# Optimization experiments

Hardware: AMD Instinct MI355X
Metric: run time of the kernel (lower is better)

The kernel has to match this reference:

```python
import jax, jax.numpy as jnp
import numpy as np

K = 64      # neighbor_num (subgraph size)
TOPK = 10   # topk for sparse adjacency scatter
DN = 10     # density_neighbor


def _build_graphs(indexes, features):
    # compute_knn: inner-product top-K neighbor table over all N samples
    N, D = features.shape
    sim = features @ features.T                      # [N, N]
    _, ori0 = jax.lax.top_k(sim, K)                  # [N, K] neighbor indices
    # density: all_sim[n] = sum_{i<DN} <f_n, f_{ori0[n,i]}> / (4*DN)
    g = features[ori0[:, :DN]]                       # [N, DN, D]
    all_sim = jnp.einsum('nd,nkd->n', features, g) / (4.0 * DN)
    exp_sim = jnp.exp(all_sim)                       # [N]

    rows = jnp.arange(K)[:, None]                    # [K,1]

    def build_one(idx):
        nbr = ori0[idx]                              # [K] neighbors of query idx
        feat = features[nbr]                         # [K, D]
        neigh = ori0[nbr][:, :TOPK]                  # [K, TOPK]
        A = (feat @ features.T) * exp_sim[None, :]   # [K, N] density-reweighted sims
        # scatter only the topk entries of each row into sparse tmp
        tmp = jnp.zeros((K, N), features.dtype).at[rows, neigh].set(A[rows, neigh])
        adj = tmp @ (tmp.T > 0).astype(features.dtype)   # [K, K]
        adj = jax.nn.softmax(adj, axis=1)
        x = feat - feat[0]                           # center on query node
        return x, adj

    return jax.vmap(build_one)(indexes)              # [B,K,D], [B,K,K]


def _gconv(x, adj, W, b):
    # GraphConv with MeanAggregator: out = relu(concat([x, adj@x]) @ W + b)
    agg = jnp.einsum('bij,bjd->bid', adj, x)
    cat = jnp.concatenate([x, agg], axis=-1)
    return jax.nn.relu(jnp.einsum('bkd,df->bkf', cat, W) + b)


def setup_inputs() -> dict:
    key = jax.random.key(0)
    ks = jax.random.split(key, 16)
    N, D, NHID = 8192, 2048, 1024
    feats = jax.random.normal(ks[0], (N, D), dtype=jnp.float32)
    feats = feats / jnp.linalg.norm(feats, axis=1, keepdims=True)  # L2-normalized embeddings
    p = lambda k, shape: jax.random.normal(k, shape, dtype=jnp.float32) * 0.02
    return {
        'indexes': jax.random.randint(ks[1], (64,), 0, N, dtype=jnp.int64) if jax.config.jax_enable_x64 else jax.random.randint(ks[1], (64,), 0, N, dtype=jnp.int32),
        'features': feats,
        'labels': jax.random.randint(ks[2], (N,), 0, 1000, dtype=jnp.int32),
        'domain': 1,
        'W1': p(ks[3], (2 * D, NHID)), 'b1': jnp.zeros((NHID,), jnp.float32),
        'W2': p(ks[4], (2 * NHID, 512)), 'b2': jnp.zeros((512,), jnp.float32),
        'W3': p(ks[5], (2 * 512, 256)), 'b3': jnp.zeros((256,), jnp.float32),
        'W4': p(ks[6], (2 * 256, 256)), 'b4': jnp.zeros((256,), jnp.float32),
        'Wc1': p(ks[7], (256, 256)), 'bc1': jnp.zeros((256,), jnp.float32),
        'prelu_a': jnp.full((256,), 0.25, jnp.float32),
        'Wc2': p(ks[8], (256, 2)), 'bc2': jnp.zeros((2,), jnp.float32),
    }


def reference(indexes, features, labels, domain, W1, b1, W2, b2, W3, b3, W4, b4,
              Wc1, bc1, prelu_a, Wc2, bc2):
    # labels only used for the (optional) loss branch; domain=1 path implemented.
    xs, adjs = _build_graphs(indexes, features)      # built under no_grad in torch
    h = _gconv(xs, adjs, W1, b1)
    h = _gconv(h, adjs, W2, b2)
    h = _gconv(h, adjs, W3, b3)
    h = _gconv(h, adjs, W4, b4)
    h = h @ Wc1 + bc1
    h = jnp.where(h > 0, h, prelu_a * h)             # PReLU(256)
    pred = h @ Wc2 + bc2                             # [B, K, 2]
    return pred
```

## Files before the change

kernel.cpp:

```cpp
#include <hip/hip_runtime.h>
#include <hip/hip_bf16.h>
#include <math.h>

#define NROWS 8192
#define DFEAT 2048
#define KSEL  64
#define CHK   2048

typedef unsigned long long u64;
typedef __attribute__((ext_vector_type(8))) short bf16x8;
typedef __attribute__((ext_vector_type(4))) float f32x4;

__device__ __forceinline__ u64 umax64(u64 a, u64 b) { return a > b ? a : b; }

__device__ __forceinline__ void split2(float v, ushort& h, ushort& l) {
  __hip_bfloat16 bh = __float2bfloat16(v);
  float r = v - __bfloat162float(bh);
  __hip_bfloat16 bl = __float2bfloat16(r);
  h = *(ushort*)&bh; l = *(ushort*)&bl;
}

__device__ __forceinline__ u64 mkkey_vi(float v, int i) {
  unsigned u = __float_as_uint(v);
  u = ((int)u < 0) ? ~u : (u | 0x80000000u);
  return ((u64)u << 32) | (u64)(0xFFFFFFFFu - (unsigned)i);
}

__global__ __launch_bounds__(256) void k_split(const float* __restrict__ F, ushort* __restrict__ H,
                                               ushort* __restrict__ M, ushort* __restrict__ L) {
  const size_t i0 = ((size_t)blockIdx.x * 256 + threadIdx.x) * 4;
  float4 x = *(const float4*)(F + i0);
  float xs[4] = {x.x, x.y, x.z, x.w};
  ushort h[4], m[4], l[4];
#pragma unroll
  for (int c = 0; c < 4; ++c) {
    float v = xs[c];
    __hip_bfloat16 bh = __float2bfloat16(v);
    float r1 = v - __bfloat162float(bh);
    __hip_bfloat16 bm = __float2bfloat16(r1);
    float r2 = r1 - __bfloat162float(bm);
    __hip_bfloat16 bl = __float2bfloat16(r2);
    h[c] = *(ushort*)&bh; m[c] = *(ushort*)&bm; l[c] = *(ushort*)&bl;
  }
  ushort4 vh = {h[0], h[1], h[2], h[3]};
  ushort4 vm = {m[0], m[1], m[2], m[3]};
  ushort4 vl = {l[0], l[1], l[2], l[3]};
  *(ushort4*)(H + i0) = vh;
  *(ushort4*)(M + i0) = vm;
  *(ushort4*)(L + i0) = vl;
}

__global__ __launch_bounds__(256) void k_simgemm_diag(
    const ushort* __restrict__ FH, const ushort* __restrict__ FM, const ushort* __restrict__ FL,
    float* __restrict__ bufbase) {
  __shared__ ushort lds[6 * 4096];
  const int cc = blockIdx.z;
  const int bj = blockIdx.x;
  const int bm = blockIdx.y;
  if (bm > bj) return;
  float* TILE = bufbase + (size_t)cc * CHK * CHK;
  const int t = threadIdx.x;
  const int w = t >> 6, l = t & 63;
  const int arow0 = cc * CHK + bm * 128;
  const int brow0 = cc * CHK + bj * 128;
  const int segr = l >> 2;
  const int segq_s = (l & 3) ^ ((l >> 3) & 3);
  const int fl15 = l & 15, fq = l >> 4;
  const int kswz = (fq ^ ((fl15 >> 1) & 3)) * 8;
  const int wr = w >> 1, wc = w & 1;
  const int mb = wr * 64, nb = wc * 64;

  f32x4 acc[4][4];
#pragma unroll
  for (int i = 0; i < 4; ++i)
#pragma unroll
    for (int j = 0; j < 4; ++j) acc[i][j] = (f32x4){0.f, 0.f, 0.f, 0.f};

  for (int k0 = 0; k0 < DFEAT; k0 += 32) {
    __syncthreads();
#pragma unroll
    for (int c = 0; c < 12; ++c) {
      const int cidx = w * 12 + c;
      const int tt = cidx >> 3;
      const int p = cidx & 7;
      const int rowbase = (tt < 3) ? arow0 : brow0;
      const int sp = (tt < 3) ? tt : (tt - 3);
      const ushort* sel = (sp == 0) ? FH : ((sp == 1) ? FM : FL);
      const ushort* g = sel + (size_t)(rowbase + p * 16 + segr) * DFEAT + (k0 + segq_s * 8);
      __builtin_amdgcn_global_load_lds((const __attribute__((address_space(1))) unsigned int*)g,
                                       (__attribute__((address_space(3))) unsigned int*)&lds[tt * 4096 + p * 512],
                                       16, 0, 0);
    }
    __syncthreads();

    bf16x8 af[3][4];
    bf16x8 bg[3][4];
#pragma unroll
    for (int i = 0; i < 3; ++i)
#pragma unroll
      for (int fm = 0; fm < 4; ++fm)
        af[i][fm] = *(const bf16x8*)&lds[i * 4096 + (mb + fm * 16 + fl15) * 32 + kswz];
#pragma unroll
    for (int j = 0; j < 3; ++j)
#pragma unroll
      for (int fn = 0; fn < 4; ++fn)
        bg[j][fn] = *(const bf16x8*)&lds[(3 + j) * 4096 + (nb + fn * 16 + fl15) * 32 + kswz];

#pragma unroll
    for (int fm = 0; fm < 4; ++fm)
#pragma unroll
      for (int fn = 0; fn < 4; ++fn) {
        f32x4 a = acc[fm][fn];
        a = __builtin_amdgcn_mfma_f32_16x16x32_bf16(af[0][fm], bg[0][fn], a, 0, 0, 0);
        a = __builtin_amdgcn_mfma_f32_16x16x32_bf16(af[1][fm], bg[0][fn], a, 0, 0, 0);
        a = __builtin_amdgcn_mfma_f32_16x16x32_bf16(af[0][fm], bg[1][fn], a, 0, 0, 0);
        a = __builtin_amdgcn_mfma_f32_16x16x32_bf16(af[2][fm], bg[0][fn], a, 0, 0, 0);
        a = __builtin_amdgcn_mfma_f32_16x16x32_bf16(af[0][fm], bg[2][fn], a, 0, 0, 0);
        a = __builtin_amdgcn_mfma_f32_16x16x32_bf16(af[1][fm], bg[1][fn], a, 0, 0, 0);
        acc[fm][fn] = a;
      }
  }

  const bool doT = (bm != bj);
#pragma unroll
  for (int fm = 0; fm < 4; ++fm) {
    const int lm = bm * 128 + mb + fm * 16 + fq * 4;
#pragma unroll
    for (int fn = 0; fn < 4; ++fn) {
      const int col = bj * 128 + nb + fn * 16 + fl15;
#pragma unroll
      for (int r = 0; r < 4; ++r)
        TILE[(size_t)(lm + r) * CHK + col] = acc[fm][fn][r];
      if (doT) {
        float4 v = make_float4(acc[fm][fn][0], acc[fm][fn][1], acc[fm][fn][2], acc[fm][fn][3]);
        *(float4*)(TILE + (size_t)col * CHK + lm) = v;
      }
    }
  }
}

__global__ __launch_bounds__(256) void k_simgemm_pair(
    const ushort* __restrict__ FH, const ushort* __restrict__ FM, const ushort* __restrict__ FL,
    float* __restrict__ T0, float* __restrict__ T0T, int i0, int j0,
    float* __restrict__ T1, float* __restrict__ T1T, int i1, int j1) {
  __shared__ ushort lds[6 * 4096];
  const int z = blockIdx.z;
  float* TILE = z ? T1 : T0;
  float* TILT = z ? T1T : T0T;
  const int ci = z ? i1 : i0;
  const int cj = z ? j1 : j0;
  const int bj = blockIdx.x;
  const int bm = blockIdx.y;
  const int t = threadIdx.x;
  const int w = t >> 6, l = t & 63;
  const int arow0 = ci * CHK + bm * 128;
  const int brow0 = cj * CHK + bj * 128;
  const int segr = l >> 2;
  const int segq_s = (l & 3) ^ ((l >> 3) & 3);
  const int fl15 = l & 15, fq = l >> 4;
  const int kswz = (fq ^ ((fl15 >> 1) & 3)) * 8;
  const int wr = w >> 1, wc = w & 1;
  const int mb = wr * 64, nb = wc * 64;

  f32x4 acc[4][4];
#pragma unroll
  for (int i = 0; i < 4; ++i)
#pragma unroll
    for (int j = 0; j < 4; ++j) acc[i][j] = (f32x4){0.f, 0.f, 0.f, 0.f};

  for (int k0 = 0; k0 < DFEAT; k0 += 32) {
    __syncthreads();
#pragma unroll
    for (int c = 0; c < 12; ++c) {
      const int cc = w * 12 + c;
      const int tt = cc >> 3;
      const int p = cc & 7;
      const int rowbase = (tt < 3) ? arow0 : brow0;
      const int sp = (tt < 3) ? tt : (tt - 3);
      const ushort* sel = (sp == 0) ? FH : ((sp == 1) ? FM : FL);
      const ushort* g = sel + (size_t)(rowbase + p * 16 + segr) * DFEAT + (k0 + segq_s * 8);
      __builtin_amdgcn_global_load_lds((const __attribute__((address_space(1))) unsigned int*)g,
                                       (__attribute__((address_space(3))) unsigned int*)&lds[tt * 4096 + p * 512],
                                       16, 0, 0);
    }
    __syncthreads();

    bf16x8 af[3][4];
    bf16x8 bg[3][4];
#pragma unroll
    for (int i = 0; i < 3; ++i)
#pragma unroll
      for (int fm = 0; fm < 4; ++fm)
        af[i][fm] = *(const bf16x8*)&lds[i * 4096 + (mb + fm * 16 + fl15) * 32 + kswz];
#pragma unroll
    for (int j = 0; j < 3; ++j)
#pragma unroll
      for (int fn = 0; fn < 4; ++fn)
        bg[j][fn] = *(const bf16x8*)&lds[(3 + j) * 4096 + (nb + fn * 16 + fl15) * 32 + kswz];

#pragma unroll
    for (int fm = 0; fm < 4; ++fm)
#pragma unroll
      for (int fn = 0; fn < 4; ++fn) {
        f32x4 a = acc[fm][fn];
        a = __builtin_amdgcn_mfma_f32_16x16x32_bf16(af[0][fm], bg[0][fn], a, 0, 0, 0);
        a = __builtin_amdgcn_mfma_f32_16x16x32_bf16(af[1][fm], bg[0][fn], a, 0, 0, 0);
        a = __builtin_amdgcn_mfma_f32_16x16x32_bf16(af[0][fm], bg[1][fn], a, 0, 0, 0);
        a = __builtin_amdgcn_mfma_f32_16x16x32_bf16(af[2][fm], bg[0][fn], a, 0, 0, 0);
        a = __builtin_amdgcn_mfma_f32_16x16x32_bf16(af[0][fm], bg[2][fn], a, 0, 0, 0);
        a = __builtin_amdgcn_mfma_f32_16x16x32_bf16(af[1][fm], bg[1][fn], a, 0, 0, 0);
        acc[fm][fn] = a;
      }
  }

#pragma unroll
  for (int fm = 0; fm < 4; ++fm) {
    const int lm = bm * 128 + mb + fm * 16 + fq * 4;
#pragma unroll
    for (int fn = 0; fn < 4; ++fn) {
      const int col = bj * 128 + nb + fn * 16 + fl15;
#pragma unroll
      for (int r = 0; r < 4; ++r)
        TILE[(size_t)(lm + r) * CHK + col] = acc[fm][fn][r];
      float4 v = make_float4(acc[fm][fn][0], acc[fm][fn][1], acc[fm][fn][2], acc[fm][fn][3]);
      *(float4*)(TILT + (size_t)col * CHK + lm) = v;
    }
  }
}

__global__ __launch_bounds__(256) void k_simgemm_mfma(
    const ushort* __restrict__ FH, const ushort* __restrict__ FM, const ushort* __restrict__ FL,
    float* __restrict__ C, int row0) {
  __shared__ ushort lds[6 * 4096];
  const int bj = blockIdx.x;
  const int bm = blockIdx.y;
  const int t = threadIdx.x;
  const int w = t >> 6, l = t & 63;
  const int arow0 = row0 + bm * 128;
  const int brow0 = bj * 128;
  const int segr = l >> 2;
  const int segq = l & 3;
  const int fl15 = l & 15, fq = l >> 4;
  const int wr = w >> 1, wc = w & 1;
  const int mb = wr * 64, nb = wc * 64;

  f32x4 acc[4][4];
#pragma unroll
  for (int i = 0; i < 4; ++i)
#pragma unroll
    for (int j = 0; j < 4; ++j) acc[i][j] = (f32x4){0.f, 0.f, 0.f, 0.f};

  for (int k0 = 0; k0 < DFEAT; k0 += 32) {
    __syncthreads();
#pragma unroll
    for (int c = 0; c < 12; ++c) {
      const int cc = w * 12 + c;
      const int tt = cc >> 3;
      const int p = cc & 7;
      const int rowbase = (tt < 3) ? arow0 : brow0;
      const int sp = (tt < 3) ? tt : (tt - 3);
      const ushort* sel = (sp == 0) ? FH : ((sp == 1) ? FM : FL);
      const ushort* g = sel + (size_t)(rowbase + p * 16 + segr) * DFEAT + (k0 + segq * 8);
      __builtin_amdgcn_global_load_lds((const __attribute__((address_space(1))) unsigned int*)g,
                                       (__attribute__((address_space(3))) unsigned int*)&lds[tt * 4096 + p * 512],
                                       16, 0, 0);
    }
    __syncthreads();

    bf16x8 af[3][4];
    bf16x8 bg[3][4];
    const int kcol = fq * 8;
#pragma unroll
    for (int i = 0; i < 3; ++i)
#pragma unroll
      for (int fm = 0; fm < 4; ++fm)
        af[i][fm] = *(const bf16x8*)&lds[i * 4096 + (mb + fm * 16 + fl15) * 32 + kcol];
#pragma unroll
    for (int j = 0; j < 3; ++j)
#pragma unroll
      for (int fn = 0; fn < 4; ++fn)
        bg[j][fn] = *(const bf16x8*)&lds[(3 + j) * 4096 + (nb + fn * 16 + fl15) * 32 + kcol];

#pragma unroll
    for (int fm = 0; fm < 4; ++fm)
#pragma unroll
      for (int fn = 0; fn < 4; ++fn) {
        f32x4 a = acc[fm][fn];
        a = __builtin_amdgcn_mfma_f32_16x16x32_bf16(af[0][fm], bg[0][fn], a, 0, 0, 0);
        a = __builtin_amdgcn_mfma_f32_16x16x32_bf16(af[1][fm], bg[0][fn], a, 0, 0, 0);
        a = __builtin_amdgcn_mfma_f32_16x16x32_bf16(af[0][fm], bg[1][fn], a, 0, 0, 0);
        a = __builtin_amdgcn_mfma_f32_16x16x32_bf16(af[2][fm], bg[0][fn], a, 0, 0, 0);
        a = __builtin_amdgcn_mfma_f32_16x16x32_bf16(af[0][fm], bg[2][fn], a, 0, 0, 0);
        a = __builtin_amdgcn_mfma_f32_16x16x32_bf16(af[1][fm], bg[1][fn], a, 0, 0, 0);
        acc[fm][fn] = a;
      }
  }

#pragma unroll
  for (int fm = 0; fm < 4; ++fm) {
    const int lm = bm * 128 + mb + fm * 16 + fq * 4;
#pragma unroll
    for (int fn = 0; fn < 4; ++fn) {
      const int col = bj * 128 + nb + fn * 16 + fl15;
#pragma unroll
      for (int r = 0; r < 4; ++r)
        C[(size_t)(lm + r) * NROWS + col] = acc[fm][fn][r];
    }
  }
}

__global__ __launch_bounds__(256) void k_gemm3(const ushort* __restrict__ AH, const ushort* __restrict__ AL,
                                               const ushort* __restrict__ BH, const ushort* __restrict__ BL,
                                               float* __restrict__ C, int K, int N) {
  __shared__ ushort lds[4 * 4096];
  const int bj = blockIdx.x, bm = blockIdx.y;
  const int t = threadIdx.x;
  const int w = t >> 6, l = t & 63;
  const int segr = l >> 2;
  const int segq_s = (l & 3) ^ ((l >> 3) & 3);
  const int fl15 = l & 15, fq = l >> 4;
  const int kswz = (fq ^ ((fl15 >> 1) & 3)) * 8;
  const int wr = w >> 1, wc = w & 1;
  const int mb = wr * 64, nb = wc * 64;

  f32x4 acc[4][4];
#pragma unroll
  for (int i = 0; i < 4; ++i)
#pragma unroll
    for (int j = 0; j < 4; ++j) acc[i][j] = (f32x4){0.f, 0.f, 0.f, 0.f};

  for (int k0 = 0; k0 < K; k0 += 32) {
    __syncthreads();
#pragma unroll
    for (int c = 0; c < 8; ++c) {
      const int s = w * 8 + c;
      const int tt = s >> 3;
      const int p = s & 7;
      const int rowbase = (tt < 2) ? (bm * 128) : (bj * 128);
      const ushort* sel = (tt == 0) ? AH : ((tt == 1) ? AL : ((tt == 2) ? BH : BL));
      const ushort* g = sel + (size_t)(rowbase + p * 16 + segr) * K + (k0 + segq_s * 8);
      __builtin_amdgcn_global_load_lds((const __attribute__((address_space(1))) unsigned int*)g,
                                       (__attribute__((address_space(3))) unsigned int*)&lds[s * 512],
                                       16, 0, 0);
    }
    __syncthreads();

    bf16x8 af[2][4];
    bf16x8 bg[2][4];
#pragma unroll
    for (int i = 0; i < 2; ++i)
#pragma unroll
      for (int fm = 0; fm < 4; ++fm)
        af[i][fm] = *(const bf16x8*)&lds[i * 4096 + (mb + fm * 16 + fl15) * 32 + kswz];
#pragma unroll
    for (int j = 0; j < 2; ++j)
#pragma unroll
      for (int fn = 0; fn < 4; ++fn)
        bg[j][fn] = *(const bf16x8*)&lds[(2 + j) * 4096 + (nb + fn * 16 + fl15) * 32 + kswz];

#pragma unroll
    for (int fm = 0; fm < 4; ++fm)
#pragma unroll
      for (int fn = 0; fn < 4; ++fn) {
        f32x4 a = acc[fm][fn];
        a = __builtin_amdgcn_mfma_f32_16x16x32_bf16(af[0][fm], bg[0][fn], a, 0, 0, 0);
        a = __builtin_amdgcn_mfma_f32_16x16x32_bf16(af[0][fm], bg[1][fn], a, 0, 0, 0);
        a = __builtin_amdgcn_mfma_f32_16x16x32_bf16(af[1][fm], bg[0][fn], a, 0, 0, 0);
        acc[fm][fn] = a;
      }
  }

#pragma unroll
  for (int fm = 0; fm < 4; ++fm) {
    const int row = bm * 128 + mb + fm * 16 + fq * 4;
#pragma unroll
    for (int fn = 0; fn < 4; ++fn) {
      const int col = bj * 128 + nb + fn * 16 + fl15;
#pragma unroll
      for (int r = 0; r < 4; ++r)
        C[(size_t)(row + r) * N + col] = acc[fm][fn][r];
    }
  }
}

__global__ __launch_bounds__(256) void k_init_topk(float* __restrict__ topv, int* __restrict__ topi) {
  const int i = blockIdx.x * 256 + threadIdx.x;
  topv[i] = -INFINITY;
  topi[i] = 0;
}

__device__ __forceinline__ void topk_merge_body(const float* src, int row, int colbase,
                                                float* topv, int* topi,
                                                unsigned* cnt, unsigned* nselp, u64* selbuf) {
  const int t = threadIdx.x;
  if (t < 64) cnt[t] = 0;
  if (t == 0) *nselp = 0;

  u64 k[9];
  int nk = 8;
#pragma unroll
  for (int q = 0; q < 8; ++q) {
    float v = src[t + 256 * q];
    k[q] = mkkey_vi(v, colbase + t + 256 * q);
  }
  k[8] = 0;
  if (t < 64) {
    k[8] = mkkey_vi(topv[(size_t)row * KSEL + t], topi[(size_t)row * KSEL + t]);
    nk = 9;
  }
  __syncthreads();

  u64 T64 = 0;
  for (int bit = 63; bit >= 0; --bit) {
    const u64 cand = T64 | (1ull << bit);
    unsigned c = 0;
#pragma unroll
    for (int q = 0; q < 9; ++q) c += (q < nk && k[q] >= cand) ? 1u : 0u;
#pragma unroll
    for (int s = 32; s > 0; s >>= 1) c += __shfl_down(c, s);
    if ((t & 63) == 0) atomicAdd(&cnt[bit], c);
    __syncthreads();
    const unsigned cb = cnt[bit];
    if (cb >= 64) T64 = cand;
    if (cb == 64) break;
  }

#pragma unroll
  for (int q = 0; q < 9; ++q) {
    if (q < nk && k[q] >= T64) {
      unsigned p = atomicAdd(nselp, 1u);
      if (p < 64) selbuf[p] = k[q];
    }
  }
  __syncthreads();

  if (t < 64) {
    u64 key = selbuf[t];
#pragma unroll
    for (int kk = 2; kk <= 64; kk <<= 1) {
#pragma unroll
      for (int j = kk >> 1; j > 0; j >>= 1) {
        u64 other = __shfl_xor(key, j);
        const bool dirDesc = ((t & kk) == 0);
        const bool upper = ((t & j) != 0);
        u64 mx = umax64(key, other);
        u64 mn = (key < other) ? key : other;
        key = (dirDesc ^ upper) ? mx : mn;
      }
    }
    const unsigned ui = (unsigned)(key >> 32);
    const float v = __uint_as_float((ui & 0x80000000u) ? (ui ^ 0x80000000u) : ~ui);
    const int idx = (int)(0xFFFFFFFFu - (unsigned)(key & 0xFFFFFFFFull));
    topv[(size_t)row * KSEL + t] = v;
    topi[(size_t)row * KSEL + t] = idx;
  }
}

__global__ __launch_bounds__(256) void k_topk_upd4(const float* __restrict__ bufbase,
                                                   int b0, int b1, int b2, int b3,
                                                   int c0, int c1, int c2, int c3,
                                                   float* __restrict__ topv, int* __restrict__ topi) {
  __shared__ unsigned cnt[64];
  __shared__ unsigned nsel;
  __shared__ u64 selbuf[64];
  const int y = blockIdx.y;
  const int bi = (y == 0) ? b0 : ((y == 1) ? b1 : ((y == 2) ? b2 : b3));
  const int cc = (y == 0) ? c0 : ((y == 1) ? c1 : ((y == 2) ? c2 : c3));
  const size_t TSZ = (size_t)CHK * CHK;
  const float* src = bufbase + (size_t)bi * TSZ + (size_t)blockIdx.x * CHK;
  topk_merge_body(src, y * CHK + blockIdx.x, cc * CHK, topv, topi, cnt, &nsel, selbuf);
}

__global__ __launch_bounds__(256) void k_exps(const float* __restrict__ topv, float* __restrict__ exps) {
  const int r = blockIdx.x * 256 + threadIdx.x;
  float s = 0.f;
#pragma unroll
  for (int q = 0; q < 10; ++q) s += topv[(size_t)r * KSEL + q];
  exps[r] = expf(s / 40.0f);
}

__global__ __launch_bounds__(256) void k_topk(const float* __restrict__ simc,
                                              float* __restrict__ topv, int* __restrict__ topi,
                                              float* __restrict__ exps, int row0) {
  __shared__ float vals[NROWS];
  __shared__ u64 wmax[4];
  __shared__ float outv[KSEL];
  __shared__ int outi[KSEL];
  const int row = row0 + blockIdx.x;
  const int t = threadIdx.x;
  const float* src = simc + (size_t)blockIdx.x * NROWS;
  for (int i = t; i < NROWS; i += 256) vals[i] = src[i];
  __syncthreads();

  u64 lk = 0;
#pragma unroll
  for (int m = 0; m < 32; ++m) {
    int i = t + 256 * m;
    lk = umax64(lk, mkkey_vi(vals[i], i));
  }

  const int lane = t & 63, wv = t >> 6;
  for (int it = 0; it < KSEL; ++it) {
    u64 wk = lk;
#pragma unroll
    for (int s = 32; s > 0; s >>= 1) {
      u64 o = __shfl_xor(wk, s);
      wk = umax64(wk, o);
    }
    if (lane == 0) wmax[wv] = wk;
    __syncthreads();
    u64 g = umax64(umax64(wmax[0], wmax[1]), umax64(wmax[2], wmax[3]));
    const unsigned ui = (unsigned)(g >> 32);
    const float v = __uint_as_float((ui & 0x80000000u) ? (ui ^ 0x80000000u) : ~ui);
    const int idx = (int)(0xFFFFFFFFu - (unsigned)(g & 0xFFFFFFFFull));
    if (t == 0) { outv[it] = v; outi[it] = idx; }
    if (t == (idx & 255)) {
      vals[idx] = -INFINITY;
      u64 nl = 0;
#pragma unroll
      for (int m = 0; m < 32; ++m) {
        int i = t + 256 * m;
        nl = umax64(nl, mkkey_vi(vals[i], i));
      }
      lk = nl;
    }
    __syncthreads();
  }
  if (t < KSEL) {
    topv[(size_t)row * KSEL + t] = outv[t];
    topi[(size_t)row * KSEL + t] = outi[t];
  }
  if (t == 0) {
    float s = 0.f;
#pragma unroll
    for (int q = 0; q < 10; ++q) s += outv[q];
    exps[row] = expf(s / 40.0f);
  }
}

__global__ __launch_bounds__(256) void k_adj(const int* __restrict__ indexes,
                                             const float* __restrict__ topv, const int* __restrict__ topi,
                                             const float* __restrict__ exps, float* __restrict__ adj) {
  __shared__ int nbr[64];
  __shared__ int neigh[64][10];
  __shared__ float tv[64][10];
  __shared__ float adjL[64][64];
  const int b = blockIdx.x;
  const int t = threadIdx.x;
  const int idx = indexes[b];
  if (t < 64) nbr[t] = topi[(size_t)idx * KSEL + t];
  __syncthreads();
  for (int p = t; p < 640; p += 256) {
    const int r = p / 10, q = p - r * 10;
    const int m = nbr[r];
    const int c = topi[(size_t)m * KSEL + q];
    neigh[r][q] = c;
    tv[r][q] = topv[(size_t)m * KSEL + q] * exps[c];
  }
  __syncthreads();
  for (int p = t; p < 4096; p += 256) {
    const int i = p >> 6, j = p & 63;
    float s = 0.f;
#pragma unroll
    for (int q = 0; q < 10; ++q) {
      const int c = neigh[i][q];
      float add = 0.f;
      for (int s2 = 0; s2 < 10; ++s2) {
        if (neigh[j][s2] == c) { add = (tv[j][s2] > 0.f) ? tv[i][q] : 0.f; break; }
      }
      s += add;
    }
    adjL[i][j] = s;
  }
  __syncthreads();
  const int wv = t >> 6, lane = t & 63;
  for (int i = wv * 16; i < wv * 16 + 16; ++i) {
    float v = adjL[i][lane];
    float mx = v;
#pragma unroll
    for (int s = 32; s > 0; s >>= 1) mx = fmaxf(mx, __shfl_xor(mx, s));
    float e = expf(v - mx);
    float sum = e;
#pragma unroll
    for (int s = 32; s > 0; s >>= 1) sum += __shfl_xor(sum, s);
    adj[((size_t)b * 64 + i) * 64 + lane] = e / sum;
  }
}

__global__ __launch_bounds__(256) void k_xs_split(const int* __restrict__ indexes, const int* __restrict__ topi,
                                                  const float* __restrict__ F,
                                                  ushort* __restrict__ XH, ushort* __restrict__ XL) {
  const int b = blockIdx.y, r = blockIdx.x;
  const int t = threadIdx.x;
  const int idx = indexes[b];
  const int m  = topi[(size_t)idx * KSEL + r];
  const int m0 = topi[(size_t)idx * KSEL + 0];
  const float4* pa = (const float4*)(F + (size_t)m * DFEAT);
  const float4* pb = (const float4*)(F + (size_t)m0 * DFEAT);
  const size_t rowoff = ((size_t)b * 64 + r) * DFEAT;
#pragma unroll
  for (int it = 0; it < 2; ++it) {
    const int i = t + it * 256;
    float4 a = pa[i], c = pb[i];
    float d[4] = {a.x - c.x, a.y - c.y, a.z - c.z, a.w - c.w};
    ushort h[4], l[4];
#pragma unroll
    for (int q = 0; q < 4; ++q) split2(d[q], h[q], l[q]);
    ushort4 vh = {h[0], h[1], h[2], h[3]};
    ushort4 vl = {l[0], l[1], l[2], l[3]};
    *(ushort4*)(XH + rowoff + i * 4) = vh;
    *(ushort4*)(XL + rowoff + i * 4) = vl;
  }
}

__global__ __launch_bounds__(256) void k_wsplitT(const float* __restrict__ W,
                                                 ushort* __restrict__ WTH, ushort* __restrict__ WTL,
                                                 int K, int F) {
  __shared__ float tile[32][33];
  const int k0 = blockIdx.x * 32;
  const int n0 = blockIdx.y * 32;
  const int t = threadIdx.x;
  {
    const int r = t >> 3, cq = t & 7;
    const int srcRow = (n0 < F) ? (k0 + r) : (K + k0 + r);
    const int srcCol = (n0 < F) ? n0 : (n0 - F);
    float4 v = *(const float4*)(W + (size_t)srcRow * F + srcCol + cq * 4);
    tile[r][cq * 4 + 0] = v.x; tile[r][cq * 4 + 1] = v.y;
    tile[r][cq * 4 + 2] = v.z; tile[r][cq * 4 + 3] = v.w;
  }
  __syncthreads();
  {
    const int nl = t >> 3, kq = t & 7;
    ushort h[4], l[4];
#pragma unroll
    for (int i = 0; i < 4; ++i) split2(tile[kq * 4 + i][nl], h[i], l[i]);
    ushort4 vh = {h[0], h[1], h[2], h[3]};
    ushort4 vl = {l[0], l[1], l[2], l[3]};
    *(ushort4*)(WTH + (size_t)(n0 + nl) * K + k0 + kq * 4) = vh;
    *(ushort4*)(WTL + (size_t)(n0 + nl) * K + k0 + kq * 4) = vl;
  }
}

__global__ __launch_bounds__(256) void k_postlayer(const float* __restrict__ C, const float* __restrict__ adj,
                                                   const float* __restrict__ bias,
                                                   ushort* __restrict__ HH, ushort* __restrict__ HL, int F) {
  __shared__ float adjL[64 * 65];
  __shared__ float QL[64 * 66];
  const int f0 = blockIdx.x * 64;
  const int b = blockIdx.y;
  const int t = threadIdx.x;
  const int fc = t & 63, rg = t >> 6;
  const int twoF = 2 * F;
  for (int i = t; i < 4096; i += 256) {
    const int r = i >> 6, j = i & 63;
    adjL[r * 65 + j] = adj[(size_t)b * 4096 + i];
    QL[r * 66 + j] = C[(size_t)(b * 64 + r) * twoF + F + f0 + j];
  }
  __syncthreads();
  const float bv = bias[f0 + fc];
  for (int rr = 0; rr < 16; ++rr) {
    const int r = rg * 16 + rr;
    float s = 0.f;
#pragma unroll 8
    for (int j0 = 0; j0 < 64; ++j0) {
      const int j = (j0 + fc) & 63;
      s += adjL[r * 65 + j] * QL[j * 66 + fc];
    }
    const int row = b * 64 + r;
    float h = C[(size_t)row * twoF + f0 + fc] + s + bv;
    h = fmaxf(h, 0.f);
    ushort hh, hl;
    split2(h, hh, hl);
    HH[(size_t)row * F + f0 + fc] = hh;
    HL[(size_t)row * F + f0 + fc] = hl;
  }
}

__global__ __launch_bounds__(256) void k_final2(const float* __restrict__ C, const float* __restrict__ bc1,
                                                const float* __restrict__ pre, const float* __restrict__ Wc2,
                                                const float* __restrict__ bc2, float* __restrict__ outp) {
  __shared__ float w[512];
  __shared__ float red[512];
  const int t = threadIdx.x;
  for (int i = t; i < 512; i += 256) w[i] = Wc2[i];
  __syncthreads();
  const int m = blockIdx.x * 64 + (t >> 2);
  const int p = t & 3;
  const float* h = C + (size_t)m * 256;
  float s0 = 0.f, s1 = 0.f;
  for (int k = p * 64; k < p * 64 + 64; ++k) {
    float hv = h[k] + bc1[k];
    hv = (hv > 0.f) ? hv : pre[k] * hv;
    s0 += hv * w[k * 2];
    s1 += hv * w[k * 2 + 1];
  }
  red[t * 2] = s0; red[t * 2 + 1] = s1;
  __syncthreads();
  if (p == 0) {
    for (int q = 1; q < 4; ++q) { s0 += red[(t + q) * 2]; s1 += red[(t + q) * 2 + 1]; }
    outp[m * 2 + 0] = s0 + bc2[0];
    outp[m * 2 + 1] = s1 + bc2[1];
  }
}

extern "C" void kernel_launch(void* const* d_in, const int* in_sizes, int n_in,
                              void* d_out, int out_size, void* d_ws, size_t ws_size,
                              hipStream_t stream) {
  const int*   indexes = (const int*)d_in[0];
  const float* F   = (const float*)d_in[1];
  const float* W1  = (const float*)d_in[4];
  const float* b1  = (const float*)d_in[5];
  const float* W2  = (const float*)d_in[6];
  const float* b2  = (const float*)d_in[7];
  const float* W3  = (const float*)d_in[8];
  const float* b3  = (const float*)d_in[9];
  const float* W4  = (const float*)d_in[10];
  const float* b4  = (const float*)d_in[11];
  const float* Wc1 = (const float*)d_in[12];
  const float* bc1 = (const float*)d_in[13];
  const float* pre = (const float*)d_in[14];
  const float* Wc2 = (const float*)d_in[15];
  const float* bc2 = (const float*)d_in[16];
  float* out = (float*)d_out;

  size_t off = 0;
  auto take = [&](size_t bytes) -> char* {
    char* q = (char*)d_ws + off;
    off += (bytes + 255) & ~(size_t)255;
    return q;
  };
  float* TOPV = (float*)take((size_t)NROWS * KSEL * 4);
  int*   TOPI = (int*)  take((size_t)NROWS * KSEL * 4);
  float* EXPS = (float*)take((size_t)NROWS * 4);
  float* ADJ  = (float*)take((size_t)64 * 64 * 64 * 4);
  char*  big  = (char*)d_ws + off;
  const size_t big_bytes = (ws_size > off) ? (ws_size - off) : 0;

  const size_t Mi = 1024 * 1024;
  const size_t Ki = 1024;
  const size_t splitBytes = (size_t)NROWS * DFEAT * 2;
  const size_t TSZ = (size_t)CHK * CHK;

  if (big_bytes >= 160 * Mi) {
    ushort* FH = (ushort*)big;
    ushort* FM = (ushort*)(big + splitBytes);
    ushort* FL = (ushort*)(big + 2 * splitBytes);
    float* BUFS = (float*)(big + 96 * Mi);
    k_split<<<NROWS * DFEAT / 1024, 256, 0, stream>>>(F, FH, FM, FL);
    k_init_topk<<<NROWS * KSEL / 256, 256, 0, stream>>>(TOPV, TOPI);
    k_simgemm_diag<<<dim3(16, 16, 4), 256, 0, stream>>>(FH, FM, FL, BUFS);
    k_topk_upd4<<<dim3(CHK, 4), 256, 0, stream>>>(BUFS, 0, 1, 2, 3, 0, 1, 2, 3, TOPV, TOPI);
    k_simgemm_pair<<<dim3(16, 16, 2), 256, 0, stream>>>(FH, FM, FL,
        BUFS + 0 * TSZ, BUFS + 1 * TSZ, 0, 1,
        BUFS + 2 * TSZ, BUFS + 3 * TSZ, 2, 3);
    k_topk_upd4<<<dim3(CHK, 4), 256, 0, stream>>>(BUFS, 0, 1, 2, 3, 1, 0, 3, 2, TOPV, TOPI);
    k_simgemm_pair<<<dim3(16, 16, 2), 256, 0, stream>>>(FH, FM, FL,
        BUFS + 0 * TSZ, BUFS + 1 * TSZ, 0, 2,
        BUFS + 2 * TSZ, BUFS + 3 * TSZ, 1, 3);
    k_topk_upd4<<<dim3(CHK, 4), 256, 0, stream>>>(BUFS, 0, 2, 1, 3, 2, 3, 0, 1, TOPV, TOPI);
    k_simgemm_pair<<<dim3(16, 16, 2), 256, 0, stream>>>(FH, FM, FL,
        BUFS + 0 * TSZ, BUFS + 1 * TSZ, 0, 3,
        BUFS + 2 * TSZ, BUFS + 3 * TSZ, 1, 2);
    k_topk_upd4<<<dim3(CHK, 4), 256, 0, stream>>>(BUFS, 0, 2, 3, 1, 3, 2, 1, 0, TOPV, TOPI);
    k_exps<<<NROWS / 256, 256, 0, stream>>>(TOPV, EXPS);
  } else {
    int fchunk = 0;
    for (int c = 2048; c >= 512; c >>= 1) {
      if (3 * splitBytes + (size_t)c * NROWS * 4 <= big_bytes) { fchunk = c; break; }
    }
    if (fchunk == 0) {
      hipMemsetAsync(d_out, 0, (size_t)out_size * 4, stream);
      return;
    }
    ushort* FH = (ushort*)big;
    ushort* FM = (ushort*)(big + splitBytes);
    ushort* FL = (ushort*)(big + 2 * splitBytes);
    float* SIMC = (float*)(big + 3 * splitBytes);
    k_split<<<NROWS * DFEAT / 1024, 256, 0, stream>>>(F, FH, FM, FL);
    for (int r0 = 0; r0 < NROWS; r0 += fchunk) {
      k_simgemm_mfma<<<dim3(64, fchunk / 128), 256, 0, stream>>>(FH, FM, FL, SIMC, r0);
      k_topk<<<fchunk, 256, 0, stream>>>(SIMC, TOPV, TOPI, EXPS, r0);
    }
  }
  k_adj<<<64, 256, 0, stream>>>(indexes, TOPV, TOPI, EXPS, ADJ);

  ushort* XH   = (ushort*)(big);
  ushort* XL   = (ushort*)(big + 16 * Mi);
  ushort* WT1H = (ushort*)(big + 32 * Mi);
  ushort* WT1L = (ushort*)(big + 40 * Mi);
  ushort* WT2H = (ushort*)(big + 48 * Mi);
  ushort* WT2L = (ushort*)(big + 50 * Mi);
  ushort* WT3H = (ushort*)(big + 52 * Mi);
  ushort* WT3L = (ushort*)(big + 52 * Mi + 512 * Ki);
  ushort* WT4H = (ushort*)(big + 53 * Mi);
  ushort* WT4L = (ushort*)(big + 53 * Mi + 256 * Ki);
  ushort* WTcH = (ushort*)(big + 53 * Mi + 512 * Ki);
  ushort* WTcL = (ushort*)(big + 53 * Mi + 640 * Ki);
  float*  CBUF = (float*)(big + 54 * Mi);
  ushort* H1H  = (ushort*)(big + 32 * Mi);
  ushort* H1L  = (ushort*)(big + 40 * Mi);
  ushort* H2H  = (ushort*)(big);
  ushort* H2L  = (ushort*)(big + 4 * Mi);
  ushort* H3H  = (ushort*)(big + 8 * Mi);
  ushort* H3L  = (ushort*)(big + 10 * Mi);
  ushort* H4H  = (ushort*)(big + 12 * Mi);
  ushort* H4L  = (ushort*)(big + 14 * Mi);

  k_wsplitT<<<dim3(2048 / 32, 2048 / 32), 256, 0, stream>>>(W1, WT1H, WT1L, 2048, 1024);
  k_wsplitT<<<dim3(1024 / 32, 1024 / 32), 256, 0, stream>>>(W2, WT2H, WT2L, 1024, 512);
  k_wsplitT<<<dim3(512 / 32, 512 / 32), 256, 0, stream>>>(W3, WT3H, WT3L, 512, 256);
  k_wsplitT<<<dim3(256 / 32, 512 / 32), 256, 0, stream>>>(W4, WT4H, WT4L, 256, 256);
  k_wsplitT<<<dim3(256 / 32, 256 / 32), 256, 0, stream>>>(Wc1, WTcH, WTcL, 256, 256);

  k_xs_split<<<dim3(64, 64), 256, 0, stream>>>(indexes, TOPI, F, XH, XL);

  k_gemm3<<<dim3(16, 32), 256, 0, stream>>>(XH, XL, WT1H, WT1L, CBUF, 2048, 2048);
  k_postlayer<<<dim3(16, 64), 256, 0, stream>>>(CBUF, ADJ, b1, H1H, H1L, 1024);
  k_gemm3<<<dim3(8, 32), 256, 0, stream>>>(H1H, H1L, WT2H, WT2L, CBUF, 1024, 1024);
  k_postlayer<<<dim3(8, 64), 256, 0, stream>>>(CBUF, ADJ, b2, H2H, H2L, 512);
  k_gemm3<<<dim3(4, 32), 256, 0, stream>>>(H2H, H2L, WT3H, WT3L, CBUF, 512, 512);
  k_postlayer<<<dim3(4, 64), 256, 0, stream>>>(CBUF, ADJ, b3, H3H, H3L, 256);
  k_gemm3<<<dim3(4, 32), 256, 0, stream>>>(H3H, H3L, WT4H, WT4L, CBUF, 256, 512);
  k_postlayer<<<dim3(4, 64), 256, 0, stream>>>(CBUF, ADJ, b4, H4H, H4L, 256);
  k_gemm3<<<dim3(2, 32), 256, 0, stream>>>(H4H, H4L, WTcH, WTcL, CBUF, 256, 256);
  k_final2<<<64, 256, 0, stream>>>(CBUF, bc1, pre, Wc2, bc2, out);
}
```

Measured before the change: 1.561 ms.

## Double-buffer LDS in split-bf16 similarity GEMM kernels to overlap loads with MFMA

```diff
diff --git a/kernel.cpp b/kernel.cpp
--- a/kernel.cpp
+++ b/kernel.cpp
@@ -53,7 +53,7 @@
 __global__ __launch_bounds__(256) void k_simgemm_diag(
     const ushort* __restrict__ FH, const ushort* __restrict__ FM, const ushort* __restrict__ FL,
     float* __restrict__ bufbase) {
-  __shared__ ushort lds[6 * 4096];
+  __shared__ ushort lds[2][6 * 4096];
   const int cc = blockIdx.z;
   const int bj = blockIdx.x;
   const int bm = blockIdx.y;
@@ -70,14 +70,7 @@
   const int wr = w >> 1, wc = w & 1;
   const int mb = wr * 64, nb = wc * 64;
 
-  f32x4 acc[4][4];
-#pragma unroll
-  for (int i = 0; i < 4; ++i)
-#pragma unroll
-    for (int j = 0; j < 4; ++j) acc[i][j] = (f32x4){0.f, 0.f, 0.f, 0.f};
-
-  for (int k0 = 0; k0 < DFEAT; k0 += 32) {
-    __syncthreads();
+  auto stage = [&](int buf, int k0) {
 #pragma unroll
     for (int c = 0; c < 12; ++c) {
       const int cidx = w * 12 + c;
@@ -88,10 +81,22 @@
       const ushort* sel = (sp == 0) ? FH : ((sp == 1) ? FM : FL);
       const ushort* g = sel + (size_t)(rowbase + p * 16 + segr) * DFEAT + (k0 + segq_s * 8);
       __builtin_amdgcn_global_load_lds((const __attribute__((address_space(1))) unsigned int*)g,
-                                       (__attribute__((address_space(3))) unsigned int*)&lds[tt * 4096 + p * 512],
+                                       (__attribute__((address_space(3))) unsigned int*)&lds[buf][tt * 4096 + p * 512],
                                        16, 0, 0);
     }
-    __syncthreads();
+  };
+
+  f32x4 acc[4][4];
+#pragma unroll
+  for (int i = 0; i < 4; ++i)
+#pragma unroll
+    for (int j = 0; j < 4; ++j) acc[i][j] = (f32x4){0.f, 0.f, 0.f, 0.f};
+
+  stage(0, 0);
+  __syncthreads();
+  int cur = 0;
+  for (int k0 = 0; k0 < DFEAT; k0 += 32) {
+    if (k0 + 32 < DFEAT) stage(cur ^ 1, k0 + 32);
 
     bf16x8 af[3][4];
     bf16x8 bg[3][4];
@@ -99,12 +104,12 @@
     for (int i = 0; i < 3; ++i)
 #pragma unroll
       for (int fm = 0; fm < 4; ++fm)
-        af[i][fm] = *(const bf16x8*)&lds[i * 4096 + (mb + fm * 16 + fl15) * 32 + kswz];
+        af[i][fm] = *(const bf16x8*)&lds[cur][i * 4096 + (mb + fm * 16 + fl15) * 32 + kswz];
 #pragma unroll
     for (int j = 0; j < 3; ++j)
 #pragma unroll
       for (int fn = 0; fn < 4; ++fn)
-        bg[j][fn] = *(const bf16x8*)&lds[(3 + j) * 4096 + (nb + fn * 16 + fl15) * 32 + kswz];
+        bg[j][fn] = *(const bf16x8*)&lds[cur][(3 + j) * 4096 + (nb + fn * 16 + fl15) * 32 + kswz];
 
 #pragma unroll
     for (int fm = 0; fm < 4; ++fm)
@@ -119,6 +124,8 @@
         a = __builtin_amdgcn_mfma_f32_16x16x32_bf16(af[1][fm], bg[1][fn], a, 0, 0, 0);
         acc[fm][fn] = a;
       }
+    __syncthreads();
+    cur ^= 1;
   }
 
   const bool doT = (bm != bj);
@@ -143,7 +150,7 @@
     const ushort* __restrict__ FH, const ushort* __restrict__ FM, const ushort* __restrict__ FL,
     float* __restrict__ T0, float* __restrict__ T0T, int i0, int j0,
     float* __restrict__ T1, float* __restrict__ T1T, int i1, int j1) {
-  __shared__ ushort lds[6 * 4096];
+  __shared__ ushort lds[2][6 * 4096];
   const int z = blockIdx.z;
   float* TILE = z ? T1 : T0;
   float* TILT = z ? T1T : T0T;
@@ -162,28 +169,33 @@
   const int wr = w >> 1, wc = w & 1;
   const int mb = wr * 64, nb = wc * 64;
 
-  f32x4 acc[4][4];
-#pragma unroll
-  for (int i = 0; i < 4; ++i)
-#pragma unroll
-    for (int j = 0; j < 4; ++j) acc[i][j] = (f32x4){0.f, 0.f, 0.f, 0.f};
-
-  for (int k0 = 0; k0 < DFEAT; k0 += 32) {
-    __syncthreads();
+  auto stage = [&](int buf, int k0) {
 #pragma unroll
     for (int c = 0; c < 12; ++c) {
-      const int cc = w * 12 + c;
-      const int tt = cc >> 3;
-      const int p = cc & 7;
+      const int cidx = w * 12 + c;
+      const int tt = cidx >> 3;
+      const int p = cidx & 7;
       const int rowbase = (tt < 3) ? arow0 : brow0;
       const int sp = (tt < 3) ? tt : (tt - 3);
       const ushort* sel = (sp == 0) ? FH : ((sp == 1) ? FM : FL);
       const ushort* g = sel + (size_t)(rowbase + p * 16 + segr) * DFEAT + (k0 + segq_s * 8);
       __builtin_amdgcn_global_load_lds((const __attribute__((address_space(1))) unsigned int*)g,
-                                       (__attribute__((address_space(3))) unsigned int*)&lds[tt * 4096 + p * 512],
+                                       (__attribute__((address_space(3))) unsigned int*)&lds[buf][tt * 4096 + p * 512],
                                        16, 0, 0);
     }
-    __syncthreads();
+  };
+
+  f32x4 acc[4][4];
+#pragma unroll
+  for (int i = 0; i < 4; ++i)
+#pragma unroll
+    for (int j = 0; j < 4; ++j) acc[i][j] = (f32x4){0.f, 0.f, 0.f, 0.f};
+
+  stage(0, 0);
+  __syncthreads();
+  int cur = 0;
+  for (int k0 = 0; k0 < DFEAT; k0 += 32) {
+    if (k0 + 32 < DFEAT) stage(cur ^ 1, k0 + 32);
 
     bf16x8 af[3][4];
     bf16x8 bg[3][4];
@@ -191,12 +203,12 @@
     for (int i = 0; i < 3; ++i)
 #pragma unroll
       for (int fm = 0; fm < 4; ++fm)
-        af[i][fm] = *(const bf16x8*)&lds[i * 4096 + (mb + fm * 16 + fl15) * 32 + kswz];
+        af[i][fm] = *(const bf16x8*)&lds[cur][i * 4096 + (mb + fm * 16 + fl15) * 32 + kswz];
 #pragma unroll
     for (int j = 0; j < 3; ++j)
 #pragma unroll
       for (int fn = 0; fn < 4; ++fn)
-        bg[j][fn] = *(const bf16x8*)&lds[(3 + j) * 4096 + (nb + fn * 16 + fl15) * 32 + kswz];
+        bg[j][fn] = *(const bf16x8*)&lds[cur][(3 + j) * 4096 + (nb + fn * 16 + fl15) * 32 + kswz];
 
 #pragma unroll
     for (int fm = 0; fm < 4; ++fm)
@@ -211,6 +223,8 @@
         a = __builtin_amdgcn_mfma_f32_16x16x32_bf16(af[1][fm], bg[1][fn], a, 0, 0, 0);
         acc[fm][fn] = a;
       }
+    __syncthreads();
+    cur ^= 1;
   }
 
 #pragma unroll
```

After: 1.959 ms. 25.5% more time.
